# Optimization experiments

Hardware: AMD Instinct MI355X
Metric: run time of the kernel (lower is better)

Reference implementation:

```python
import jax, jax.numpy as jnp
import numpy as np

N_NODES = 100000
N_EDGES = 3200000
IN_CH = 128
HID = 64
N_GRAPHS = 512


def _gcn_conv(x, W, b, src, dst, n_nodes):
    """PyG GCNConv: out = D^{-1/2} (A + I) D^{-1/2} X W + b.
    src/dst are edge endpoints; self-loops handled analytically."""
    h = x @ W  # [N, out]
    # degree with self-loops (count at target nodes, as in PyG)
    deg = jnp.zeros((n_nodes,), h.dtype).at[dst].add(1.0) + 1.0
    dis = jax.lax.rsqrt(deg)  # deg^{-1/2}
    norm = dis[src] * dis[dst]  # [E]
    msg = h[src] * norm[:, None]  # gather + scale, [E, out]
    out = jnp.zeros_like(h).at[dst].add(msg)  # scatter-add
    # self-loop term: norm_ii = 1/deg_i
    out = out + h * (dis * dis)[:, None]
    return out + b


def setup_inputs() -> dict:
    key = jax.random.key(0)
    ks = jax.random.split(key, 8)
    x = jax.random.normal(ks[0], (N_NODES, IN_CH), dtype=jnp.float32)
    edge_index = jax.random.randint(ks[1], (2, N_EDGES), 0, N_NODES, dtype=jnp.int64)
    batch = jnp.sort(jax.random.randint(ks[2], (N_NODES,), 0, N_GRAPHS, dtype=jnp.int64))
    s1 = 1.0 / np.sqrt(IN_CH)
    s2 = 1.0 / np.sqrt(HID)
    W1 = jax.random.uniform(ks[3], (IN_CH, HID), jnp.float32, -s1, s1)
    b1 = jax.random.uniform(ks[4], (HID,), jnp.float32, -s1, s1)
    W2 = jax.random.uniform(ks[5], (HID, HID), jnp.float32, -s2, s2)
    b2 = jax.random.uniform(ks[6], (HID,), jnp.float32, -s2, s2)
    return {"x": x, "edge_index": edge_index, "batch": batch,
            "W1": W1, "b1": b1, "W2": W2, "b2": b2}


def reference(x, edge_index, batch, W1, b1, W2, b2):
    src, dst = edge_index[0], edge_index[1]
    n = x.shape[0]
    h = jax.nn.relu(_gcn_conv(x, W1, b1, src, dst, n))
    h = jax.nn.relu(_gcn_conv(h, W2, b2, src, dst, n))
    # F.dropout(p=0.2) treated as identity (eval / deterministic reference)
    # global_mean_pool: segment mean over graph ids
    sums = jax.ops.segment_sum(h, batch, num_segments=N_GRAPHS)
    cnts = jax.ops.segment_sum(jnp.ones((n,), h.dtype), batch, num_segments=N_GRAPHS)
    return sums / jnp.maximum(cnts, 1.0)[:, None]
```

## Files before the change

### kernel.cpp

```cpp
#include <hip/hip_runtime.h>

typedef unsigned int uint;
typedef float f32x2 __attribute__((ext_vector_type(2)));

#define N_NODES 100000
#define N_EDGES 3200000
#define IN_CH 128
#define HID 64
#define N_GRAPHS 512
#define EPB 4096
#define NBLK ((N_EDGES + EPB - 1) / EPB)
#define NB 391
#define CAP 10240

__device__ __forceinline__ uint f2bf1(float f) {
    union { float f; uint i; } v; v.f = f;
    return (v.i + 0x7fffu + ((v.i >> 16) & 1u)) >> 16;
}
__device__ __forceinline__ uint pack2(float lo, float hi) {
    return f2bf1(lo) | (f2bf1(hi) << 16);
}
__device__ __forceinline__ float2 ub2(uint u) {
    union { uint i; float f; } a, b;
    a.i = u << 16; b.i = u & 0xffff0000u;
    return make_float2(a.f, b.f);
}
__device__ __forceinline__ f32x2 up2(uint u) {
    union { uint i; float f; } lo, hi;
    lo.i = u << 16; hi.i = u & 0xffff0000u;
    f32x2 r; r.x = lo.f; r.y = hi.f;
    return r;
}

__global__ __launch_bounds__(256) void scatter_kernel(const int* __restrict__ src,
                                                      const int* __restrict__ dst,
                                                      int* __restrict__ bcnt,
                                                      uint* __restrict__ pairs) {
    __shared__ int h[4 * NB];
    __shared__ int start[NB];
    __shared__ int cur[NB];
    int t = threadIdx.x;
    int base = blockIdx.x * EPB;

    int rs[16], rd[16];
#pragma unroll
    for (int j = 0; j < 16; ++j) {
        int e = base + j * 256 + t;
        if (e < N_EDGES) { rs[j] = src[e]; rd[j] = dst[e]; }
        else rd[j] = -1;
    }
    for (int i = t; i < 4 * NB; i += 256) h[i] = 0;
    __syncthreads();
    int w = t >> 6;
#pragma unroll
    for (int j = 0; j < 16; ++j)
        if (rd[j] >= 0) atomicAdd(&h[w * NB + (rd[j] >> 8)], 1);
    __syncthreads();
    for (int b = t; b < NB; b += 256) {
        int tot = h[b] + h[NB + b] + h[2 * NB + b] + h[3 * NB + b];
        start[b] = tot ? atomicAdd(&bcnt[b * 16], tot) : 0;
        cur[b] = 0;
    }
    __syncthreads();
#pragma unroll
    for (int j = 0; j < 16; ++j) {
        if (rd[j] >= 0) {
            int b = rd[j] >> 8;
            int r = atomicAdd(&cur[b], 1);
            pairs[(size_t)b * CAP + start[b] + r] =
                ((uint)(rd[j] & 255) << 24) | (uint)rs[j];
        }
    }
}

__global__ __launch_bounds__(512) void bucket_csr_kernel(const uint* __restrict__ pairs,
                                                         const int* __restrict__ bcnt,
                                                         int* __restrict__ csr_src,
                                                         int* __restrict__ rstart,
                                                         int* __restrict__ rend,
                                                         float* __restrict__ dis) {
    __shared__ int h8[8 * 256];
    __shared__ int h[256];
    int b = blockIdx.x;
    int t = threadIdx.x;
    int w = t >> 6;
    int e0 = b * CAP;
    int e1 = e0 + bcnt[b * 16];

    for (int i = t; i < 8 * 256; i += 512) h8[i] = 0;
    __syncthreads();

    int* hw = &h8[w * 256];
    int e = e0 + t;
    for (; e + 1536 < e1; e += 2048) {
        uint p0 = pairs[e], p1 = pairs[e + 512], p2 = pairs[e + 1024], p3 = pairs[e + 1536];
        atomicAdd(&hw[p0 >> 24], 1);
        atomicAdd(&hw[p1 >> 24], 1);
        atomicAdd(&hw[p2 >> 24], 1);
        atomicAdd(&hw[p3 >> 24], 1);
    }
    for (; e < e1; e += 512)
        atomicAdd(&hw[pairs[e] >> 24], 1);
    __syncthreads();

    int v = 0;
    if (t < 256) {
#pragma unroll
        for (int j = 0; j < 8; ++j) v += h8[j * 256 + t];
        h[t] = v;
    }
    __syncthreads();
#pragma unroll
    for (int o = 1; o < 256; o <<= 1) {
        int x = (t >= o && t < 256) ? h[t - o] : 0;
        __syncthreads();
        if (t < 256) h[t] += x;
        __syncthreads();
    }
    int excl = (t < 256) ? h[t] - v : 0;
    int n = b * 256 + t;
    if (t < 256 && n < N_NODES) {
        rstart[n] = e0 + excl;
        rend[n] = e0 + excl + v;
        dis[n] = rsqrtf((float)v + 1.0f);
    }
    __syncthreads();
    if (t < 256) h[t] = e0 + excl;
    __syncthreads();

    e = e0 + t;
    for (; e + 1536 < e1; e += 2048) {
        uint p0 = pairs[e], p1 = pairs[e + 512], p2 = pairs[e + 1024], p3 = pairs[e + 1536];
        int q0 = atomicAdd(&h[p0 >> 24], 1);
        int q1 = atomicAdd(&h[p1 >> 24], 1);
        int q2 = atomicAdd(&h[p2 >> 24], 1);
        int q3 = atomicAdd(&h[p3 >> 24], 1);
        csr_src[q0] = (int)(p0 & 0xFFFFFFu);
        csr_src[q1] = (int)(p1 & 0xFFFFFFu);
        csr_src[q2] = (int)(p2 & 0xFFFFFFu);
        csr_src[q3] = (int)(p3 & 0xFFFFFFu);
    }
    for (; e < e1; e += 512) {
        uint p = pairs[e];
        int pos = atomicAdd(&h[p >> 24], 1);
        csr_src[pos] = (int)(p & 0xFFFFFFu);
    }
}

__global__ __launch_bounds__(256) void gemm1_kernel(const float* __restrict__ X,
                                                    const float* __restrict__ W,
                                                    const float* __restrict__ dis,
                                                    uint* __restrict__ Y) {
    __shared__ float Wl[IN_CH * 64];
    __shared__ float Xs[128 * 33];
    int t = threadIdx.x;
    for (int idx = t; idx < IN_CH * 64; idx += 256) Wl[idx] = W[idx];

    int r0 = (t >> 3) * 4;
    int c0 = (t & 7) * 8;
    int rowBase = blockIdx.x * 128;

    float acc[4][8];
#pragma unroll
    for (int a = 0; a < 4; ++a)
#pragma unroll
        for (int c = 0; c < 8; ++c) acc[a][c] = 0.f;

    int srow = t >> 1;
    int shh = (t & 1) * 16;
    bool sok = (rowBase + srow) < N_NODES;
    const float* xbase = X + (size_t)(rowBase + srow) * IN_CH + shh;

    float4 nx[4];
#pragma unroll
    for (int f = 0; f < 4; ++f)
        nx[f] = sok ? *reinterpret_cast<const float4*>(xbase + f * 4)
                    : make_float4(0.f, 0.f, 0.f, 0.f);

    for (int kc = 0; kc < IN_CH; kc += 32) {
        if (kc) __syncthreads();
#pragma unroll
        for (int f = 0; f < 4; ++f) {
            int o = srow * 33 + shh + f * 4;
            Xs[o] = nx[f].x; Xs[o + 1] = nx[f].y; Xs[o + 2] = nx[f].z; Xs[o + 3] = nx[f].w;
        }
        __syncthreads();
        if (kc + 32 < IN_CH) {
#pragma unroll
            for (int f = 0; f < 4; ++f)
                nx[f] = sok ? *reinterpret_cast<const float4*>(xbase + kc + 32 + f * 4)
                            : make_float4(0.f, 0.f, 0.f, 0.f);
        }
#pragma unroll
        for (int kk = 0; kk < 32; ++kk) {
            const float4 wa = *reinterpret_cast<const float4*>(&Wl[(kc + kk) * 64 + c0]);
            const float4 wb = *reinterpret_cast<const float4*>(&Wl[(kc + kk) * 64 + c0 + 4]);
            float xr[4];
#pragma unroll
            for (int a = 0; a < 4; ++a) xr[a] = Xs[(r0 + a) * 33 + kk];
#pragma unroll
            for (int a = 0; a < 4; ++a) {
                acc[a][0] += xr[a] * wa.x; acc[a][1] += xr[a] * wa.y;
                acc[a][2] += xr[a] * wa.z; acc[a][3] += xr[a] * wa.w;
                acc[a][4] += xr[a] * wb.x; acc[a][5] += xr[a] * wb.y;
                acc[a][6] += xr[a] * wb.z; acc[a][7] += xr[a] * wb.w;
            }
        }
    }
#pragma unroll
    for (int a = 0; a < 4; ++a) {
        int row = rowBase + r0 + a;
        if (row < N_NODES) {
            float d = dis[row];
            uint4 o;
            o.x = pack2(acc[a][0] * d, acc[a][1] * d);
            o.y = pack2(acc[a][2] * d, acc[a][3] * d);
            o.z = pack2(acc[a][4] * d, acc[a][5] * d);
            o.w = pack2(acc[a][6] * d, acc[a][7] * d);
            *reinterpret_cast<uint4*>(Y + (size_t)row * 32 + (t & 7) * 4) = o;
        }
    }
}

__global__ __launch_bounds__(256) void gemm2_kernel(const uint* __restrict__ X,
                                                    const float* __restrict__ W,
                                                    const float* __restrict__ dis,
                                                    uint* __restrict__ Y) {
    __shared__ float Wl[HID * 64];
    __shared__ float Xs[128 * 33];
    int t = threadIdx.x;
    for (int idx = t; idx < HID * 64; idx += 256) Wl[idx] = W[idx];

    int r0 = (t >> 3) * 4;
    int c0 = (t & 7) * 8;
    int rowBase = blockIdx.x * 128;

    float acc[4][8];
#pragma unroll
    for (int a = 0; a < 4; ++a)
#pragma unroll
        for (int c = 0; c < 8; ++c) acc[a][c] = 0.f;

    int srow = t >> 1;
    int shh = (t & 1) * 16;
    bool sok = (rowBase + srow) < N_NODES;
    const uint* xbase = X + (size_t)(rowBase + srow) * 32 + (t & 1) * 8;

    uint4 n0_ = make_uint4(0, 0, 0, 0), n1_ = n0_;
    if (sok) {
        n0_ = *reinterpret_cast<const uint4*>(xbase);
        n1_ = *reinterpret_cast<const uint4*>(xbase + 4);
    }

    for (int kc = 0; kc < HID; kc += 32) {
        if (kc) __syncthreads();
        {
            uint us[8] = {n0_.x, n0_.y, n0_.z, n0_.w, n1_.x, n1_.y, n1_.z, n1_.w};
            int o = srow * 33 + shh;
#pragma unroll
            for (int j = 0; j < 8; ++j) {
                float2 f = ub2(us[j]);
                Xs[o + 2 * j]     = fmaxf(f.x, 0.f);
                Xs[o + 2 * j + 1] = fmaxf(f.y, 0.f);
            }
        }
        __syncthreads();
        if (kc + 32 < HID && sok) {
            n0_ = *reinterpret_cast<const uint4*>(xbase + 16);
            n1_ = *reinterpret_cast<const uint4*>(xbase + 20);
        }
#pragma unroll
        for (int kk = 0; kk < 32; ++kk) {
            const float4 wa = *reinterpret_cast<const float4*>(&Wl[(kc + kk) * 64 + c0]);
            const float4 wb = *reinterpret_cast<const float4*>(&Wl[(kc + kk) * 64 + c0 + 4]);
            float xr[4];
#pragma unroll
            for (int a = 0; a < 4; ++a) xr[a] = Xs[(r0 + a) * 33 + kk];
#pragma unroll
            for (int a = 0; a < 4; ++a) {
                acc[a][0] += xr[a] * wa.x; acc[a][1] += xr[a] * wa.y;
                acc[a][2] += xr[a] * wa.z; acc[a][3] += xr[a] * wa.w;
                acc[a][4] += xr[a] * wb.x; acc[a][5] += xr[a] * wb.y;
                acc[a][6] += xr[a] * wb.z; acc[a][7] += xr[a] * wb.w;
            }
        }
    }
#pragma unroll
    for (int a = 0; a < 4; ++a) {
        int row = rowBase + r0 + a;
        if (row < N_NODES) {
            float d = dis[row];
            uint4 o;
            o.x = pack2(acc[a][0] * d, acc[a][1] * d);
            o.y = pack2(acc[a][2] * d, acc[a][3] * d);
            o.z = pack2(acc[a][4] * d, acc[a][5] * d);
            o.w = pack2(acc[a][6] * d, acc[a][7] * d);
            *reinterpret_cast<uint4*>(Y + (size_t)row * 32 + (t & 7) * 4) = o;
        }
    }
}

__global__ __launch_bounds__(256) void gather_kernel(const int* __restrict__ rstart,
                                                     const int* __restrict__ rend,
                                                     const int* __restrict__ csr_src,
                                                     const float* __restrict__ dis,
                                                     const float* __restrict__ bias,
                                                     const uint* __restrict__ A,
                                                     uint* __restrict__ B) {
    int i = blockIdx.x * 4 + (threadIdx.x >> 6);
    if (i >= N_NODES) return;
    int lane = threadIdx.x & 63;
    int q = lane >> 3;
    int cu = (lane & 7) * 4;

    float4 bi0 = *reinterpret_cast<const float4*>(&bias[(lane & 7) * 8]);
    float4 bi1 = *reinterpret_cast<const float4*>(&bias[(lane & 7) * 8 + 4]);

    int e = rstart[i];
    int end = rend[i];

    f32x2 a[4], b[4];
#pragma unroll
    for (int j = 0; j < 4; ++j) { a[j] = (f32x2)0.f; b[j] = (f32x2)0.f; }

    if (q == 0) {
        uint4 u = *reinterpret_cast<const uint4*>(&A[(size_t)i * 32 + cu]);
        a[0] += up2(u.x); a[1] += up2(u.y); a[2] += up2(u.z); a[3] += up2(u.w);
    }
    for (; e + 16 <= end; e += 16) {
        int s0 = csr_src[e + q];
        int s1 = csr_src[e + 8 + q];
        uint4 u0 = *reinterpret_cast<const uint4*>(&A[(size_t)s0 * 32 + cu]);
        uint4 u1 = *reinterpret_cast<const uint4*>(&A[(size_t)s1 * 32 + cu]);
        a[0] += up2(u0.x); a[1] += up2(u0.y); a[2] += up2(u0.z); a[3] += up2(u0.w);
        b[0] += up2(u1.x); b[1] += up2(u1.y); b[2] += up2(u1.z); b[3] += up2(u1.w);
    }
    for (; e + 8 <= end; e += 8) {
        int s = csr_src[e + q];
        uint4 u = *reinterpret_cast<const uint4*>(&A[(size_t)s * 32 + cu]);
        a[0] += up2(u.x); a[1] += up2(u.y); a[2] += up2(u.z); a[3] += up2(u.w);
    }
    if (e + q < end) {
        int s = csr_src[e + q];
        uint4 u = *reinterpret_cast<const uint4*>(&A[(size_t)s * 32 + cu]);
        b[0] += up2(u.x); b[1] += up2(u.y); b[2] += up2(u.z); b[3] += up2(u.w);
    }
    float r[8];
#pragma unroll
    for (int j = 0; j < 4; ++j) {
        f32x2 s = a[j] + b[j];
        r[2 * j] = s.x; r[2 * j + 1] = s.y;
    }
#pragma unroll
    for (int j = 0; j < 8; ++j) {
        r[j] += __shfl_xor(r[j], 8);
        r[j] += __shfl_xor(r[j], 16);
        r[j] += __shfl_xor(r[j], 32);
    }
    if (q == 0) {
        float d = dis[i];
        uint4 o;
        o.x = pack2(bi0.x + d * r[0], bi0.y + d * r[1]);
        o.y = pack2(bi0.z + d * r[2], bi0.w + d * r[3]);
        o.z = pack2(bi1.x + d * r[4], bi1.y + d * r[5]);
        o.w = pack2(bi1.z + d * r[6], bi1.w + d * r[7]);
        *reinterpret_cast<uint4*>(B + (size_t)i * 32 + (lane & 7) * 4) = o;
    }
}

__global__ __launch_bounds__(256) void pool_kernel(const uint* __restrict__ B,
                                                   const int* __restrict__ batch,
                                                   float* __restrict__ sums,
                                                   float* __restrict__ cnt) {
    int w = blockIdx.x * 4 + (threadIdx.x >> 6);
    int half = (threadIdx.x >> 5) & 1;
    int l = threadIdx.x & 31;
    int n0 = w * 32 + half * 16;
    if (n0 >= N_NODES) return;
    int n1 = min(n0 + 16, N_NODES);
    int curg = batch[n0];
    float a0 = 0.f, a1 = 0.f;
    int run = 0;
    for (int n = n0; n < n1; ++n) {
        int g = batch[n];
        if (g != curg) {
            atomicAdd(&sums[curg * 64 + 2 * l], a0);
            atomicAdd(&sums[curg * 64 + 2 * l + 1], a1);
            if (l == 0) atomicAdd(&cnt[curg], (float)run);
            curg = g; a0 = 0.f; a1 = 0.f; run = 0;
        }
        float2 f = ub2(B[(size_t)n * 32 + l]);
        a0 += fmaxf(f.x, 0.f);
        a1 += fmaxf(f.y, 0.f);
        run++;
    }
    atomicAdd(&sums[curg * 64 + 2 * l], a0);
    atomicAdd(&sums[curg * 64 + 2 * l + 1], a1);
    if (l == 0) atomicAdd(&cnt[curg], (float)run);
}

__global__ __launch_bounds__(256) void final_kernel(const float* __restrict__ sums,
                                                    const float* __restrict__ cnt,
                                                    float* __restrict__ out) {
    int idx = blockIdx.x * 256 + threadIdx.x;
    if (idx < N_GRAPHS * 64) out[idx] = sums[idx] / fmaxf(cnt[idx >> 6], 1.0f);
}

extern "C" void kernel_launch(void* const* d_in, const int* in_sizes, int n_in,
                              void* d_out, int out_size, void* d_ws, size_t ws_size,
                              hipStream_t stream) {
    const float* x     = (const float*)d_in[0];
    const int*   edge  = (const int*)d_in[1];
    const int*   batch = (const int*)d_in[2];
    const float* W1    = (const float*)d_in[3];
    const float* b1    = (const float*)d_in[4];
    const float* W2    = (const float*)d_in[5];
    const float* b2    = (const float*)d_in[6];
    float* out = (float*)d_out;

    uint*  A        = (uint*)d_ws;
    uint*  B        = A + (size_t)N_NODES * 32;
    uint*  pairs    = B + (size_t)N_NODES * 32;
    int*   csr_src  = (int*)(pairs + (size_t)NB * CAP);
    float* dis      = (float*)(csr_src + (size_t)NB * CAP);
    int*   rstart   = (int*)(dis + N_NODES);
    int*   rend     = rstart + N_NODES;
    float* sums     = (float*)(rend + N_NODES);
    float* cnt_f    = sums + (size_t)N_GRAPHS * 64;
    int*   bcnt     = (int*)(cnt_f + N_GRAPHS);

    const int* src = edge;
    const int* dst = edge + N_EDGES;

    hipMemsetAsync(sums, 0, (N_GRAPHS * 64 + N_GRAPHS + NB * 16) * sizeof(float), stream);

    scatter_kernel<<<NBLK, 256, 0, stream>>>(src, dst, bcnt, pairs);
    bucket_csr_kernel<<<NB, 512, 0, stream>>>(pairs, bcnt, csr_src, rstart, rend, dis);

    gemm1_kernel<<<(N_NODES + 127) / 128, 256, 0, stream>>>(x, W1, dis, A);
    gather_kernel<<<(N_NODES + 3) / 4, 256, 0, stream>>>(rstart, rend, csr_src, dis, b1, A, B);

    gemm2_kernel<<<(N_NODES + 127) / 128, 256, 0, stream>>>(B, W2, dis, A);
    gather_kernel<<<(N_NODES + 3) / 4, 256, 0, stream>>>(rstart, rend, csr_src, dis, b2, A, B);

    pool_kernel<<<(N_NODES + 127) / 128, 256, 0, stream>>>(B, batch, sums, cnt_f);
    final_kernel<<<(N_GRAPHS * 64 + 255) / 256, 256, 0, stream>>>(sums, cnt_f, out);
}
```

Measured before the change: 357.5 us.

## Stage scatter pairs in LDS for coalesced writes; fuse pooling into second gather

The edge scatter kernel now computes a block-local prefix scan over bucket counts, sorts each block's pairs into a shared-memory staging buffer, and writes them out contiguously by bucket. The goal is coalesced global stores in place of random scattered ones. The second gather kernel is templated to apply ReLU and atomically accumulate per-graph sums and counts directly, which removes the separate pool kernel and the bf16 round trip of the final hidden layer. The cost is more shared memory and a 9-step scan with barriers in the scatter kernel, plus one global float atomic per node per channel, and these atomics may contend on the same graph rows.

```diff
diff --git a/kernel.cpp b/kernel.cpp
--- a/kernel.cpp
+++ b/kernel.cpp
@@ -1,6 +1,7 @@
 #include <hip/hip_runtime.h>
 
 typedef unsigned int uint;
+typedef unsigned short ushort;
 typedef float f32x2 __attribute__((ext_vector_type(2)));
 
 #define N_NODES 100000
@@ -36,9 +37,12 @@
                                                       const int* __restrict__ dst,
                                                       int* __restrict__ bcnt,
                                                       uint* __restrict__ pairs) {
-    __shared__ int h[4 * NB];
-    __shared__ int start[NB];
+    __shared__ int h4[4 * NB];
+    __shared__ int gbase[NB];
     __shared__ int cur[NB];
+    __shared__ int scan[512];
+    __shared__ uint stage[EPB];
+    __shared__ ushort sbid[EPB];
     int t = threadIdx.x;
     int base = blockIdx.x * EPB;
 
@@ -49,28 +53,50 @@
         if (e < N_EDGES) { rs[j] = src[e]; rd[j] = dst[e]; }
         else rd[j] = -1;
     }
-    for (int i = t; i < 4 * NB; i += 256) h[i] = 0;
+    for (int i = t; i < 4 * NB; i += 256) h4[i] = 0;
     __syncthreads();
     int w = t >> 6;
 #pragma unroll
     for (int j = 0; j < 16; ++j)
-        if (rd[j] >= 0) atomicAdd(&h[w * NB + (rd[j] >> 8)], 1);
-    __syncthreads();
+        if (rd[j] >= 0) atomicAdd(&h4[w * NB + (rd[j] >> 8)], 1);
+    __syncthreads();
+
+    for (int b = t; b < 512; b += 256)
+        scan[b] = (b < NB) ? (h4[b] + h4[NB + b] + h4[2 * NB + b] + h4[3 * NB + b]) : 0;
+    __syncthreads();
+#pragma unroll
+    for (int o = 1; o < 512; o <<= 1) {
+        int a0 = (t >= o) ? scan[t - o] : 0;
+        int a1 = (t + 256 >= o) ? scan[t + 256 - o] : 0;
+        __syncthreads();
+        scan[t] += a0;
+        scan[t + 256] += a1;
+        __syncthreads();
+    }
+
     for (int b = t; b < NB; b += 256) {
-        int tot = h[b] + h[NB + b] + h[2 * NB + b] + h[3 * NB + b];
-        start[b] = tot ? atomicAdd(&bcnt[b * 16], tot) : 0;
-        cur[b] = 0;
-    }
-    __syncthreads();
+        int cnt = h4[b] + h4[NB + b] + h4[2 * NB + b] + h4[3 * NB + b];
+        int loff = scan[b] - cnt;
+        int start = cnt ? atomicAdd(&bcnt[b * 16], cnt) : 0;
+        gbase[b] = b * CAP + start - loff;
+        cur[b] = loff;
+    }
+    __syncthreads();
+
 #pragma unroll
     for (int j = 0; j < 16; ++j) {
         if (rd[j] >= 0) {
             int b = rd[j] >> 8;
             int r = atomicAdd(&cur[b], 1);
-            pairs[(size_t)b * CAP + start[b] + r] =
-                ((uint)(rd[j] & 255) << 24) | (uint)rs[j];
-        }
-    }
+            stage[r] = ((uint)(rd[j] & 255) << 24) | (uint)rs[j];
+            sbid[r] = (ushort)b;
+        }
+    }
+    __syncthreads();
+
+    int total = scan[NB - 1];
+    for (int i = t; i < total; i += 256)
+        pairs[(size_t)gbase[sbid[i]] + i] = stage[i];
 }
 
 __global__ __launch_bounds__(512) void bucket_csr_kernel(const uint* __restrict__ pairs,
@@ -300,13 +326,17 @@
     }
 }
 
+template <bool POOL>
 __global__ __launch_bounds__(256) void gather_kernel(const int* __restrict__ rstart,
                                                      const int* __restrict__ rend,
                                                      const int* __restrict__ csr_src,
                                                      const float* __restrict__ dis,
                                                      const float* __restrict__ bias,
                                                      const uint* __restrict__ A,
-                                                     uint* __restrict__ B) {
+                                                     uint* __restrict__ B,
+                                                     const int* __restrict__ batch,
+                                                     float* __restrict__ sums,
+                                                     float* __restrict__ cnt) {
     int i = blockIdx.x * 4 + (threadIdx.x >> 6);
     if (i >= N_NODES) return;
     int lane = threadIdx.x & 63;
@@ -359,44 +389,27 @@
     }
     if (q == 0) {
         float d = dis[i];
-        uint4 o;
-        o.x = pack2(bi0.x + d * r[0], bi0.y + d * r[1]);
-        o.y = pack2(bi0.z + d * r[2], bi0.w + d * r[3]);
-        o.z = pack2(bi1.x + d * r[4], bi1.y + d * r[5]);
-        o.w = pack2(bi1.z + d * r[6], bi1.w + d * r[7]);
-        *reinterpret_cast<uint4*>(B + (size_t)i * 32 + (lane & 7) * 4) = o;
-    }
-}
-
-__global__ __launch_bounds__(256) void pool_kernel(const uint* __restrict__ B,
-                                                   const int* __restrict__ batch,
-                                                   float* __restrict__ sums,
-                                                   float* __restrict__ cnt) {
-    int w = blockIdx.x * 4 + (threadIdx.x >> 6);
-    int half = (threadIdx.x >> 5) & 1;
-    int l = threadIdx.x & 31;
-    int n0 = w * 32 + half * 16;
-    if (n0 >= N_NODES) return;
-    int n1 = min(n0 + 16, N_NODES);
-    int curg = batch[n0];
-    float a0 = 0.f, a1 = 0.f;
-    int run = 0;
-    for (int n = n0; n < n1; ++n) {
-        int g = batch[n];
-        if (g != curg) {
-            atomicAdd(&sums[curg * 64 + 2 * l], a0);
-            atomicAdd(&sums[curg * 64 + 2 * l + 1], a1);
-            if (l == 0) atomicAdd(&cnt[curg], (float)run);
-            curg = g; a0 = 0.f; a1 = 0.f; run = 0;
-        }
-        float2 f = ub2(B[(size_t)n * 32 + l]);
-        a0 += fmaxf(f.x, 0.f);
-        a1 += fmaxf(f.y, 0.f);
-        run++;
-    }
-    atomicAdd(&sums[curg * 64 + 2 * l], a0);
-    atomicAdd(&sums[curg * 64 + 2 * l + 1], a1);
-    if (l == 0) atomicAdd(&cnt[curg], (float)run);
+        if (!POOL) {
+            uint4 o;
+            o.x = pack2(bi0.x + d * r[0], bi0.y + d * r[1]);
+            o.y = pack2(bi0.z + d * r[2], bi0.w + d * r[3]);
+            o.z = pack2(bi1.x + d * r[4], bi1.y + d * r[5]);
+            o.w = pack2(bi1.z + d * r[6], bi1.w + d * r[7]);
+            *reinterpret_cast<uint4*>(B + (size_t)i * 32 + (lane & 7) * 4) = o;
+        } else {
+            int gr = batch[i];
+            float* sb = &sums[gr * 64 + (lane & 7) * 8];
+            atomicAdd(&sb[0], fmaxf(bi0.x + d * r[0], 0.f));
+            atomicAdd(&sb[1], fmaxf(bi0.y + d * r[1], 0.f));
+            atomicAdd(&sb[2], fmaxf(bi0.z + d * r[2], 0.f));
+            atomicAdd(&sb[3], fmaxf(bi0.w + d * r[3], 0.f));
+            atomicAdd(&sb[4], fmaxf(bi1.x + d * r[4], 0.f));
+            atomicAdd(&sb[5], fmaxf(bi1.y + d * r[5], 0.f));
+            atomicAdd(&sb[6], fmaxf(bi1.z + d * r[6], 0.f));
+            atomicAdd(&sb[7], fmaxf(bi1.w + d * r[7], 0.f));
+            if (lane == 0) atomicAdd(&cnt[gr], 1.0f);
+        }
+    }
 }
 
 __global__ __launch_bounds__(256) void final_kernel(const float* __restrict__ sums,
@@ -438,11 +451,12 @@
     bucket_csr_kernel<<<NB, 512, 0, stream>>>(pairs, bcnt, csr_src, rstart, rend, dis);
 
     gemm1_kernel<<<(N_NODES + 127) / 128, 256, 0, stream>>>(x, W1, dis, A);
-    gather_kernel<<<(N_NODES + 3) / 4, 256, 0, stream>>>(rstart, rend, csr_src, dis, b1, A, B);
+    gather_kernel<false><<<(N_NODES + 3) / 4, 256, 0, stream>>>(
+        rstart, rend, csr_src, dis, b1, A, B, batch, sums, cnt_f);
 
     gemm2_kernel<<<(N_NODES + 127) / 128, 256, 0, stream>>>(B, W2, dis, A);
-    gather_kernel<<<(N_NODES + 3) / 4, 256, 0, stream>>>(rstart, rend, csr_src, dis, b2, A, B);
-
-    pool_kernel<<<(N_NODES + 127) / 128, 256, 0, stream>>>(B, batch, sums, cnt_f);
+    gather_kernel<true><<<(N_NODES + 3) / 4, 256, 0, stream>>>(
+        rstart, rend, csr_src, dis, b2, A, B, batch, sums, cnt_f);
+
     final_kernel<<<(N_GRAPHS * 64 + 255) / 256, 256, 0, stream>>>(sums, cnt_f, out);
 }
```

New measurement: 686.3 us. +92.0%, slower.

## Stage scatter pairs in shared memory sorted by bucket for coalesced writes

Applied to the files above, without the earlier changes.

The edge scatter kernel now computes a block-local prefix scan over bucket counts, places each packed pair into a shared-memory staging buffer ordered by bucket, and then writes the staged pairs to global memory in contiguous runs. This replaces scattered per-edge global stores with mostly coalesced ones. The cost is extra shared memory (about 24KB more), a 9-step scan with barriers, and an extra pass through LDS, which may lower occupancy.

```diff
diff --git a/kernel.cpp b/kernel.cpp
--- a/kernel.cpp
+++ b/kernel.cpp
@@ -1,6 +1,7 @@
 #include <hip/hip_runtime.h>
 
 typedef unsigned int uint;
+typedef unsigned short ushort;
 typedef float f32x2 __attribute__((ext_vector_type(2)));
 
 #define N_NODES 100000
@@ -36,9 +37,12 @@
                                                       const int* __restrict__ dst,
                                                       int* __restrict__ bcnt,
                                                       uint* __restrict__ pairs) {
-    __shared__ int h[4 * NB];
-    __shared__ int start[NB];
+    __shared__ int h4[4 * NB];
+    __shared__ int gbase[NB];
     __shared__ int cur[NB];
+    __shared__ int scan[512];
+    __shared__ uint stage[EPB];
+    __shared__ ushort sbid[EPB];
     int t = threadIdx.x;
     int base = blockIdx.x * EPB;
 
@@ -49,28 +53,50 @@
         if (e < N_EDGES) { rs[j] = src[e]; rd[j] = dst[e]; }
         else rd[j] = -1;
     }
-    for (int i = t; i < 4 * NB; i += 256) h[i] = 0;
+    for (int i = t; i < 4 * NB; i += 256) h4[i] = 0;
     __syncthreads();
     int w = t >> 6;
 #pragma unroll
     for (int j = 0; j < 16; ++j)
-        if (rd[j] >= 0) atomicAdd(&h[w * NB + (rd[j] >> 8)], 1);
-    __syncthreads();
+        if (rd[j] >= 0) atomicAdd(&h4[w * NB + (rd[j] >> 8)], 1);
+    __syncthreads();
+
+    for (int b = t; b < 512; b += 256)
+        scan[b] = (b < NB) ? (h4[b] + h4[NB + b] + h4[2 * NB + b] + h4[3 * NB + b]) : 0;
+    __syncthreads();
+#pragma unroll
+    for (int o = 1; o < 512; o <<= 1) {
+        int a0 = (t >= o) ? scan[t - o] : 0;
+        int a1 = (t + 256 >= o) ? scan[t + 256 - o] : 0;
+        __syncthreads();
+        scan[t] += a0;
+        scan[t + 256] += a1;
+        __syncthreads();
+    }
+
     for (int b = t; b < NB; b += 256) {
-        int tot = h[b] + h[NB + b] + h[2 * NB + b] + h[3 * NB + b];
-        start[b] = tot ? atomicAdd(&bcnt[b * 16], tot) : 0;
-        cur[b] = 0;
-    }
-    __syncthreads();
+        int cnt = h4[b] + h4[NB + b] + h4[2 * NB + b] + h4[3 * NB + b];
+        int loff = scan[b] - cnt;
+        int start = cnt ? atomicAdd(&bcnt[b * 16], cnt) : 0;
+        gbase[b] = b * CAP + start - loff;
+        cur[b] = loff;
+    }
+    __syncthreads();
+
 #pragma unroll
     for (int j = 0; j < 16; ++j) {
         if (rd[j] >= 0) {
             int b = rd[j] >> 8;
             int r = atomicAdd(&cur[b], 1);
-            pairs[(size_t)b * CAP + start[b] + r] =
-                ((uint)(rd[j] & 255) << 24) | (uint)rs[j];
-        }
-    }
+            stage[r] = ((uint)(rd[j] & 255) << 24) | (uint)rs[j];
+            sbid[r] = (ushort)b;
+        }
+    }
+    __syncthreads();
+
+    int total = scan[NB - 1];
+    for (int i = t; i < total; i += 256)
+        pairs[(size_t)gbase[sbid[i]] + i] = stage[i];
 }
 
 __global__ __launch_bounds__(512) void bucket_csr_kernel(const uint* __restrict__ pairs,
```

New measurement: 348.8 us. -2.4%, faster.
